# Kernel tuning notes

Hardware: AMD Instinct MI355X
Metric: run time of the kernel (lower is better)

The kernel has to match this reference:

```python
import jax, jax.numpy as jnp
import numpy as np

SIDE = 64; EMB = 16; CH = 64; K = 64; V = 64; L = 8
N = SIDE * SIDE

def _pos_table(side, d):
    pe = np.array([[p / np.power(10000, 2 * (j // 2) / d) for j in range(d)]
                   if p != 0 else np.zeros(d) for p in range(side)])
    pe[1:, 0::2] = np.sin(pe[1:, 0::2])
    pe[1:, 1::2] = np.cos(pe[1:, 1::2])
    return pe.astype(np.float32)  # [side, d]

def _pos_emb():
    # Replicates torch .view(1, emb, side, 1): plain reshape of [side, emb] -> [emb, side]
    t = _pos_table(SIDE, EMB).reshape(EMB, SIDE)
    xe = np.broadcast_to(t[:, :, None], (EMB, SIDE, SIDE))
    ye = np.broadcast_to(t[:, None, :], (EMB, SIDE, SIDE))
    return jnp.asarray(np.concatenate([xe, ye], 0).reshape(1, 2 * EMB, N))

def _conv_mask():
    # CausalConv mask, see_center=False, 5x5: zero center pixel onward in center row, and all rows below
    m = np.ones((CH, 3, 5, 5), np.float32)
    m[:, :, 2, 2:] = 0.0
    m[:, :, 3:, :] = 0.0
    return jnp.asarray(m)

def _lrelu(x):
    return jnp.where(x >= 0, x, 0.01 * x)  # LeakyReLU(0.01)

def _bn(x, g, b, eps=1e-5):
    # training-mode batch norm (biased variance), channel axis = 1
    axes = (0,) + tuple(range(2, x.ndim))
    m = jnp.mean(x, axes, keepdims=True)
    var = jnp.mean((x - m) ** 2, axes, keepdims=True)
    sh = (1, -1) + (1,) * (x.ndim - 2)
    return g.reshape(sh) * (x - m) / jnp.sqrt(var + eps) + b.reshape(sh)

def _cv1(w, b, x):
    # 1x1 Conv1d: [O,I] x [B,I,N] -> [B,O,N]
    return jnp.einsum('oi,bin->bon', w, x) + b[:, None]

def reference(x, conv_w, conv_b, bn0_g, bn0_b, q_w, q_b, fk_w, fk_b, ck_w, ck_b,
              fv_w, fv_b, cv_w, cv_b, bn_g, bn_b, out_w, out_b):
    B = x.shape[0]
    pos = jnp.broadcast_to(_pos_emb(), (B, 2 * EMB, N))
    mask = jnp.tril(jnp.ones((N, N), jnp.float32))

    # masked causal conv input layer + BN + LeakyReLU
    w = conv_w * _conv_mask()
    h = jax.lax.conv_general_dilated(x, w, (1, 1), [(2, 2), (2, 2)],
                                     dimension_numbers=('NCHW', 'OIHW', 'NCHW'))
    h = h + conv_b[None, :, None, None]
    h = _lrelu(_bn(h, bn0_g, bn0_b)).reshape(B, CH, N)

    k0 = jnp.zeros((B, K, N), x.dtype)
    v0 = jnp.zeros((B, V, N), x.dtype)
    inv_sqrt_k = 1.0 / jnp.sqrt(jnp.float32(K))

    def layer(carry, p):
        h, k, v = carry
        qw, qb, fkw, fkb, ckw, ckb, fvw, fvb, cvw, cvb, g, bb = p
        x0 = jnp.concatenate([h, pos], 1)            # [B, CH+32, N]
        x0k = jnp.concatenate([x0, k], 1)            # [B, 160, N]
        x0v = jnp.concatenate([x0, v], 1)
        fk = jax.nn.sigmoid(_cv1(fkw, fkb, x0k))
        ck = _lrelu(_cv1(ckw, ckb, x0k))
        k_new = fk * k + ck                          # highway-gated persistent K
        fv = jax.nn.sigmoid(_cv1(fvw, fvb, x0v))
        cv_ = _lrelu(_cv1(cvw, cvb, x0v))
        v_new = fv * v + cv_
        q = _lrelu(_cv1(qw, qb, x0))                 # [B, K, N]
        attn = jnp.einsum('bkn,bkm->bnm', q, k) * inv_sqrt_k  # uses OLD k
        attn = attn * mask + (1.0 - mask) * (-10000.0)
        attn = jax.nn.softmax(attn, axis=-1) * mask
        out1 = jnp.einsum('bnm,bvm->bvn', attn, v)   # uses OLD v; [B, V, N]
        # original code computes fc(out1) but discards it (out2 overwritten)
        h2 = _lrelu(_bn(out1, g, bb))
        return (h2, k_new, v_new), None

    params = (q_w, q_b, fk_w, fk_b, ck_w, ck_b, fv_w, fv_b, cv_w, cv_b, bn_g, bn_b)
    (h, k, v), _ = jax.lax.scan(layer, (h, k0, v0), params)

    out = jnp.einsum('oi,bin->bon', out_w, h) + out_b[None, :, None]
    return out.reshape(B, out_w.shape[0], SIDE, SIDE)

def setup_inputs() -> dict:
    key = jax.random.key(0)
    ks = jax.random.split(key, 12)
    s = 0.05
    return {
        'x': jax.random.normal(ks[0], (2, 3, 64, 64), jnp.float32),
        'conv_w': jax.random.normal(ks[1], (CH, 3, 5, 5), jnp.float32) * s,
        'conv_b': jnp.zeros((CH,), jnp.float32),
        'bn0_g': jnp.ones((CH,), jnp.float32),
        'bn0_b': jnp.zeros((CH,), jnp.float32),
        'q_w': jax.random.normal(ks[2], (L, K, CH + 2 * EMB), jnp.float32) * s,
        'q_b': jnp.zeros((L, K), jnp.float32),
        'fk_w': jax.random.normal(ks[3], (L, K, CH + K + 2 * EMB), jnp.float32) * s,
        'fk_b': jnp.zeros((L, K), jnp.float32),
        'ck_w': jax.random.normal(ks[4], (L, K, CH + K + 2 * EMB), jnp.float32) * s,
        'ck_b': jnp.zeros((L, K), jnp.float32),
        'fv_w': jax.random.normal(ks[5], (L, V, CH + V + 2 * EMB), jnp.float32) * s,
        'fv_b': jnp.zeros((L, V), jnp.float32),
        'cv_w': jax.random.normal(ks[6], (L, V, CH + V + 2 * EMB), jnp.float32) * s,
        'cv_b': jnp.zeros((L, V), jnp.float32),
        'bn_g': jnp.ones((L, CH), jnp.float32),
        'bn_b': jnp.zeros((L, CH), jnp.float32),
        'out_w': jax.random.normal(ks[7], (100, V), jnp.float32) * s,
        'out_b': jnp.zeros((100,), jnp.float32),
    }
```

## Files before the change

kernel.cpp:

```cpp
#include <hip/hip_runtime.h>

#define NPIX 4096
#define CHN  64

typedef __attribute__((ext_vector_type(8))) short short8;
typedef __attribute__((ext_vector_type(8))) unsigned short ushort8;
typedef __attribute__((ext_vector_type(4))) unsigned short ushort4v;
typedef __attribute__((ext_vector_type(4))) float f32x4;

__device__ __forceinline__ float lrelu_(float x){ return x >= 0.f ? x : 0.01f*x; }

__device__ __forceinline__ unsigned short f2bf(float x){
  union { float f; unsigned u; } v; v.f = x;
  unsigned r = v.u + 0x7FFF + ((v.u >> 16) & 1);
  return (unsigned short)(r >> 16);
}
__device__ __forceinline__ float bf2f(unsigned short h){
  union { unsigned u; float f; } v; v.u = ((unsigned)h) << 16;
  return v.f;
}

__global__ void pos_kernel(float* __restrict__ pos){
  int idx = blockIdx.x*256 + threadIdx.x;
  int c = idx >> 12;
  int n = idx & (NPIX-1);
  int bcoord = (c < 16) ? (n >> 6) : (n & 63);
  int a = (c < 16) ? c : (c - 16);
  int flat = a*64 + bcoord;
  int p = flat >> 4;
  int j = flat & 15;
  float val = 0.f;
  if (p != 0){
    float ex = (float)(j & ~1) * (1.f/16.f);
    float w = powf(10000.f, -ex);
    float ang = (float)p * w;
    val = (j & 1) ? cosf(ang) : sinf(ang);
  }
  pos[idx] = val;
}

__global__ void wtr_kernel(const float* __restrict__ qw, const float* __restrict__ fkw,
                           const float* __restrict__ ckw, const float* __restrict__ fvw,
                           const float* __restrict__ cvw, const float* __restrict__ convw,
                           float* __restrict__ wt){
  int idx = blockIdx.x*256 + threadIdx.x;
  if (idx >= 381632) return;
  if (idx < 49152){
    int l = idx / 6144, r = idx % 6144, i = r >> 6, o = r & 63;
    wt[idx] = qw[(l*64 + o)*96 + i];
  } else if (idx < 376832){
    int e = idx - 49152;
    int mat = e / 81920, r = e % 81920;
    int l = r / 10240, rr = r % 10240, i = rr >> 6, o = rr & 63;
    const float* src = (mat==0) ? fkw : (mat==1) ? ckw : (mat==2) ? fvw : cvw;
    wt[idx] = src[(l*64 + o)*160 + i];
  } else {
    int e = idx - 376832;
    int o = e & 63, tap = e >> 6;
    int ci = tap / 25, r = tap % 25;
    wt[idx] = convw[(o*3 + ci)*25 + r];
  }
}

__global__ __launch_bounds__(256) void conv_in_kernel(const float* __restrict__ x,
                                                      const float* __restrict__ cwt,
                                                      const float* __restrict__ cb,
                                                      float* __restrict__ out){
  int t = threadIdx.x;
  int o = t & 63;
  int sub = t >> 6;
  int bid = blockIdx.x;
  int b = bid >> 10;
  int n = ((bid & 1023) << 2) + sub;
  int y = n >> 6, xx = n & 63;
  float acc = cb[o];
  #pragma unroll
  for (int ci=0; ci<3; ++ci){
    const float* xp = x + ((b*3+ci)<<12);
    #pragma unroll
    for (int ky=0; ky<3; ++ky){
      int yy = y + ky - 2;
      if (yy < 0) continue;
      int nk = (ky==2) ? 2 : 5;
      #pragma unroll
      for (int kx=0; kx<5; ++kx){
        if (kx >= nk) break;
        int xc = xx + kx - 2;
        if (xc < 0 || xc > 63) continue;
        acc += xp[(yy<<6) + xc] * cwt[(ci*25 + ky*5 + kx)*64 + o];
      }
    }
  }
  out[(b*CHN+o)*NPIX + n] = acc;
}

__global__ __launch_bounds__(1024) void bn_stats_kernel(const float* __restrict__ xin,
                                                        float* __restrict__ stats){
  int c = blockIdx.x;
  int t = threadIdx.x;
  float s = 0.f, ss = 0.f;
  #pragma unroll
  for (int it=0; it<8; ++it){
    int idx = t + it*1024;
    float v = xin[(((idx>>12))*CHN + c)*NPIX + (idx & (NPIX-1))];
    s += v; ss += v*v;
  }
  #pragma unroll
  for (int o=1; o<64; o<<=1){ s += __shfl_xor(s,o); ss += __shfl_xor(ss,o); }
  __shared__ float ps[16], pq[16];
  if ((t & 63) == 0){ ps[t>>6] = s; pq[t>>6] = ss; }
  __syncthreads();
  if (t == 0){
    float S=0.f, Q=0.f;
    #pragma unroll
    for (int i=0;i<16;++i){ S += ps[i]; Q += pq[i]; }
    float mu = S*(1.f/8192.f);
    float var = Q*(1.f/8192.f) - mu*mu;
    var = fmaxf(var, 0.f);
    stats[c*2]   = mu;
    stats[c*2+1] = rsqrtf(var + 1e-5f);
  }
}

__global__ void bn_apply_kernel(const float* __restrict__ xin, const float* __restrict__ stats,
                                const float* __restrict__ g, const float* __restrict__ bb,
                                float* __restrict__ hout){
  int idx = blockIdx.x*256 + threadIdx.x;
  int e = idx << 2;
  int c = (e >> 12) & 63;
  float mu = stats[c*2], rstd = stats[c*2+1];
  float gain = g[c]*rstd;
  float beta = bb[c] - gain*mu;
  float4 v = *(const float4*)(xin + e);
  float4 r;
  r.x = lrelu_(gain*v.x + beta);
  r.y = lrelu_(gain*v.y + beta);
  r.z = lrelu_(gain*v.z + beta);
  r.w = lrelu_(gain*v.w + beta);
  *(float4*)(hout + e) = r;
}

__global__ __launch_bounds__(256) void bn_apply2_kernel(const float* __restrict__ xin,
                                                        const float* __restrict__ psum,
                                                        const float* __restrict__ psq,
                                                        const float* __restrict__ g,
                                                        const float* __restrict__ bb,
                                                        float* __restrict__ hout){
  int bid = blockIdx.x;
  int ebase = bid << 10;
  int c = (ebase >> 12) & 63;
  int t = threadIdx.x;
  float s = psum[c*256 + t];
  float q = psq[c*256 + t];
  #pragma unroll
  for (int o=1; o<64; o<<=1){ s += __shfl_xor(s,o); q += __shfl_xor(q,o); }
  __shared__ float as[4], aq[4];
  if ((t & 63) == 0){ as[t>>6] = s; aq[t>>6] = q; }
  __syncthreads();
  float S = as[0]+as[1]+as[2]+as[3];
  float Q = aq[0]+aq[1]+aq[2]+aq[3];
  float mu = S*(1.f/8192.f);
  float var = fmaxf(Q*(1.f/8192.f) - mu*mu, 0.f);
  float rstd = rsqrtf(var + 1e-5f);
  float gain = g[c]*rstd;
  float beta = bb[c] - gain*mu;
  float4 v = *(const float4*)(xin + ebase + t*4);
  float4 r;
  r.x = lrelu_(gain*v.x + beta);
  r.y = lrelu_(gain*v.y + beta);
  r.z = lrelu_(gain*v.z + beta);
  r.w = lrelu_(gain*v.w + beta);
  *(float4*)(hout + ebase + t*4) = r;
}

__global__ __launch_bounds__(256) void cv1_kernel(
    const float* __restrict__ hbuf, const float* __restrict__ pos,
    const float* __restrict__ kold, const float* __restrict__ vold,
    const float* __restrict__ qwt,
    const float* __restrict__ fkwt, const float* __restrict__ ckwt,
    const float* __restrict__ fvwt, const float* __restrict__ cvwt,
    const float* __restrict__ qbi,  const float* __restrict__ fkb,
    const float* __restrict__ ckb,  const float* __restrict__ fvb,
    const float* __restrict__ cvb,
    unsigned short* __restrict__ qh, unsigned short* __restrict__ ql,
    float* __restrict__ knew, unsigned short* __restrict__ khn, unsigned short* __restrict__ kln,
    float* __restrict__ vnew, unsigned short* __restrict__ vhTn, unsigned short* __restrict__ vlTn)
{
  int t = threadIdx.x;
  int o  = t & 63;
  int wv = t >> 6;
  int b    = blockIdx.x >> 8;
  int tile = blockIdx.x & 255;
  int n0 = tile*16 + wv*4;

  const float* hb = hbuf + b*CHN*NPIX + n0;
  const float* kb = kold + b*CHN*NPIX + n0;
  const float* vb = vold + b*CHN*NPIX + n0;
  const float* pb = pos + n0;

  auto load4 = [&](const float* p, float* dst){
    float4 a = *(const float4*)p;
    dst[0]=a.x; dst[1]=a.y; dst[2]=a.z; dst[3]=a.w;
  };

  float x[4];
  long obase = (long)(b*CHN+o)*NPIX + n0;
  size_t nbase = ((size_t)b*NPIX + n0)*64 + o;

  {
    float aq[4];
    float bias = qbi[o];
    #pragma unroll
    for (int j=0;j<4;++j) aq[j]=bias;
    #pragma unroll 4
    for (int i=0;i<64;++i){
      load4(hb + i*NPIX, x);
      float w = qwt[i*64 + o];
      #pragma unroll
      for (int j=0;j<4;++j) aq[j] += w*x[j];
    }
    #pragma unroll 4
    for (int i=0;i<32;++i){
      load4(pb + i*NPIX, x);
      float w = qwt[(64+i)*64 + o];
      #pragma unroll
      for (int j=0;j<4;++j) aq[j] += w*x[j];
    }
    #pragma unroll
    for (int j=0;j<4;++j){
      float v = lrelu_(aq[j]) * 0.125f;
      unsigned short hb16 = f2bf(v);
      qh[nbase + (size_t)j*64] = hb16;
      ql[nbase + (size_t)j*64] = f2bf(v - bf2f(hb16));
    }
  }

  {
    float af[4], ac[4];
    float bf = fkb[o], bc = ckb[o];
    #pragma unroll
    for (int j=0;j<4;++j){ af[j]=bf; ac[j]=bc; }
    #pragma unroll 4
    for (int i=0;i<64;++i){
      load4(hb + i*NPIX, x);
      float wf = fkwt[i*64+o], wc = ckwt[i*64+o];
      #pragma unroll
      for (int j=0;j<4;++j){ af[j] += wf*x[j]; ac[j] += wc*x[j]; }
    }
    #pragma unroll 4
    for (int i=0;i<32;++i){
      load4(pb + i*NPIX, x);
      float wf = fkwt[(64+i)*64+o], wc = ckwt[(64+i)*64+o];
      #pragma unroll
      for (int j=0;j<4;++j){ af[j] += wf*x[j]; ac[j] += wc*x[j]; }
    }
    #pragma unroll 4
    for (int i=0;i<64;++i){
      load4(kb + i*NPIX, x);
      float wf = fkwt[(96+i)*64+o], wc = ckwt[(96+i)*64+o];
      #pragma unroll
      for (int j=0;j<4;++j){ af[j] += wf*x[j]; ac[j] += wc*x[j]; }
    }
    float kv[4];
    load4(kb + o*NPIX, kv);
    #pragma unroll
    for (int j=0;j<4;++j){
      float fk = 1.f/(1.f+__expf(-af[j]));
      float kn = fk*kv[j] + lrelu_(ac[j]);
      knew[obase+j] = kn;
      unsigned short hb16 = f2bf(kn);
      khn[nbase + (size_t)j*64] = hb16;
      kln[nbase + (size_t)j*64] = f2bf(kn - bf2f(hb16));
    }
  }

  {
    float af[4], ac[4];
    float bf = fvb[o], bc = cvb[o];
    #pragma unroll
    for (int j=0;j<4;++j){ af[j]=bf; ac[j]=bc; }
    #pragma unroll 4
    for (int i=0;i<64;++i){
      load4(hb + i*NPIX, x);
      float wf = fvwt[i*64+o], wc = cvwt[i*64+o];
      #pragma unroll
      for (int j=0;j<4;++j){ af[j] += wf*x[j]; ac[j] += wc*x[j]; }
    }
    #pragma unroll 4
    for (int i=0;i<32;++i){
      load4(pb + i*NPIX, x);
      float wf = fvwt[(64+i)*64+o], wc = cvwt[(64+i)*64+o];
      #pragma unroll
      for (int j=0;j<4;++j){ af[j] += wf*x[j]; ac[j] += wc*x[j]; }
    }
    #pragma unroll 4
    for (int i=0;i<64;++i){
      load4(vb + i*NPIX, x);
      float wf = fvwt[(96+i)*64+o], wc = cvwt[(96+i)*64+o];
      #pragma unroll
      for (int j=0;j<4;++j){ af[j] += wf*x[j]; ac[j] += wc*x[j]; }
    }
    float vv[4];
    load4(vb + o*NPIX, vv);
    ushort4v vph, vpl;
    #pragma unroll
    for (int j=0;j<4;++j){
      float fv = 1.f/(1.f+__expf(-af[j]));
      float vn = fv*vv[j] + lrelu_(ac[j]);
      vnew[obase+j] = vn;
      unsigned short hb16 = f2bf(vn);
      vph[j] = hb16;
      vpl[j] = f2bf(vn - bf2f(hb16));
    }
    *(ushort4v*)(vhTn + ((size_t)(b*CHN+o))*NPIX + n0) = vph;
    *(ushort4v*)(vlTn + ((size_t)(b*CHN+o))*NPIX + n0) = vpl;
  }
}

__global__ __launch_bounds__(128) void attn_mfma(
    const unsigned short* __restrict__ qhg, const unsigned short* __restrict__ qlg,
    const unsigned short* __restrict__ khg, const unsigned short* __restrict__ klg,
    const unsigned short* __restrict__ vhg, const unsigned short* __restrict__ vlg,
    float* __restrict__ part)
{
  int bid = 639 - (int)blockIdx.x;
  int b = 0, id = bid;
  if (id >= 320){ b = 1; id -= 320; }
  int pidx = bid;
  int rem = id, k = 0;
  while (rem >= 32*(k+1)){ rem -= 32*(k+1); ++k; }
  int rt    = 32*k + rem/(k+1);
  int chunk = rem - (rem/(k+1))*(k+1);

  int C0  = chunk << 10;
  int end = min(C0 + 1024, rt*32 + 32);
  int nt  = (end - C0 + 63) >> 6;

  int t = threadIdx.x;
  int w = t >> 6;
  int l = t & 63;
  int r = l & 15;
  int g = l >> 4;
  int n_g = rt*32 + w*16 + r;

  __shared__ __align__(16) char KH[8192], KL[8192];
  __shared__ __align__(16) char VH[8192], VL[8192];
  __shared__ __align__(16) char PH[2][2048], PL[2][2048];

  const unsigned short* qhp = qhg + (size_t)b*NPIX*64;
  const unsigned short* qlp = qlg + (size_t)b*NPIX*64;
  const unsigned short* khp = khg + (size_t)b*NPIX*64;
  const unsigned short* klp = klg + (size_t)b*NPIX*64;
  const unsigned short* vhp = vhg + (size_t)b*CHN*NPIX;
  const unsigned short* vlp = vlg + (size_t)b*CHN*NPIX;

  short8 qh0 = *(const short8*)(qhp + (size_t)n_g*64 + 8*g);
  short8 qh1 = *(const short8*)(qhp + (size_t)n_g*64 + 8*g + 32);
  short8 ql0 = *(const short8*)(qlp + (size_t)n_g*64 + 8*g);
  short8 ql1 = *(const short8*)(qlp + (size_t)n_g*64 + 8*g + 32);

  int srow[4], scc8[4], soff[4];
  #pragma unroll
  for (int p=0; p<4; ++p){
    int slot = t + (p<<7);
    int row = slot >> 3, cc = slot & 7;
    srow[p] = row; scc8[p] = cc*8;
    soff[p] = row*128 + ((cc ^ (row & 7)) << 4);
  }

  ushort8 rkh[4], rkl[4], rvh[4], rvl[4];
  auto issue = [&](int m0){
    #pragma unroll
    for (int p=0; p<4; ++p){
      rkh[p] = *(const ushort8*)(khp + (size_t)(m0+srow[p])*64 + scc8[p]);
      rkl[p] = *(const ushort8*)(klp + (size_t)(m0+srow[p])*64 + scc8[p]);
      rvh[p] = *(const ushort8*)(vhp + (size_t)srow[p]*NPIX + m0 + scc8[p]);
      rvl[p] = *(const ushort8*)(vlp + (size_t)srow[p]*NPIX + m0 + scc8[p]);
    }
  };

  f32x4 zero4 = {0.f,0.f,0.f,0.f};
  f32x4 oacc[4];
  #pragma unroll
  for (int vf=0; vf<4; ++vf) oacc[vf] = zero4;
  float m_run = -1e30f, l_run = 0.f;

  int nmax_w = rt*32 + w*16 + 15;

  issue(C0);
  for (int ti=0; ti<nt; ++ti){
    int m0 = C0 + (ti<<6);
    __syncthreads();
    #pragma unroll
    for (int p=0; p<4; ++p){
      *(ushort8*)(KH + soff[p]) = rkh[p];
      *(ushort8*)(KL + soff[p]) = rkl[p];
      *(ushort8*)(VH + soff[p]) = rvh[p];
      *(ushort8*)(VL + soff[p]) = rvl[p];
    }
    __syncthreads();
    if (ti+1 < nt) issue(m0 + 64);

    if (m0 <= nmax_w){
      f32x4 sf[4];
      #pragma unroll
      for (int mf=0; mf<4; ++mf) sf[mf] = zero4;
      #pragma unroll
      for (int kc=0; kc<2; ++kc){
        short8 qfh = kc ? qh1 : qh0;
        short8 qfl = kc ? ql1 : ql0;
        int ch = ((g + 4*kc) ^ (r & 7)) << 4;
        #pragma unroll
        for (int mf=0; mf<4; ++mf){
          int ro = (16*mf + r)*128;
          short8 ah = *(const short8*)(KH + ro + ch);
          short8 al = *(const short8*)(KL + ro + ch);
          sf[mf] = __builtin_amdgcn_mfma_f32_16x16x32_bf16(ah, qfh, sf[mf], 0,0,0);
          sf[mf] = __builtin_amdgcn_mfma_f32_16x16x32_bf16(al, qfh, sf[mf], 0,0,0);
          sf[mf] = __builtin_amdgcn_mfma_f32_16x16x32_bf16(ah, qfl, sf[mf], 0,0,0);
        }
      }
      float pv[16];
      float mx = -1e30f;
      #pragma unroll
      for (int mf=0; mf<4; ++mf){
        #pragma unroll
        for (int q2=0; q2<4; ++q2){
          int mg = m0 + 16*mf + 4*g + q2;
          float s = sf[mf][q2];
          s = (mg <= n_g) ? s : -1e30f;
          pv[mf*4+q2] = s;
          mx = fmaxf(mx, s);
        }
      }
      mx = fmaxf(mx, __shfl_xor(mx, 16));
      mx = fmaxf(mx, __shfl_xor(mx, 32));
      float m_new = fmaxf(m_run, mx);
      float alpha = __expf(m_run - m_new);
      float ps = 0.f;
      #pragma unroll
      for (int i=0; i<16; ++i){ pv[i] = __expf(pv[i] - m_new); ps += pv[i]; }
      ps += __shfl_xor(ps, 16);
      ps += __shfl_xor(ps, 32);
      l_run = l_run*alpha + ps;
      m_run = m_new;

      #pragma unroll
      for (int mf=0; mf<4; ++mf){
        unsigned short h_[4], l_[4];
        #pragma unroll
        for (int q2=0; q2<4; ++q2){
          float xv = pv[mf*4+q2];
          h_[q2] = f2bf(xv);
          l_[q2] = f2bf(xv - bf2f(h_[q2]));
        }
        int addr = r*128 + ((((g>>1) + 2*mf) ^ (r & 7)) << 4) + ((g&1)<<3);
        uint2 wh = make_uint2((unsigned)h_[0] | ((unsigned)h_[1]<<16),
                              (unsigned)h_[2] | ((unsigned)h_[3]<<16));
        uint2 wl = make_uint2((unsigned)l_[0] | ((unsigned)l_[1]<<16),
                              (unsigned)l_[2] | ((unsigned)l_[3]<<16));
        *(uint2*)(PH[w] + addr) = wh;
        *(uint2*)(PL[w] + addr) = wl;
      }
      #pragma unroll
      for (int vf=0; vf<4; ++vf) oacc[vf] *= alpha;

      #pragma unroll
      for (int kc=0; kc<2; ++kc){
        int ch = ((g + 4*kc) ^ (r & 7)) << 4;
        short8 pfh = *(const short8*)(PH[w] + r*128 + ch);
        short8 pfl = *(const short8*)(PL[w] + r*128 + ch);
        #pragma unroll
        for (int vf=0; vf<4; ++vf){
          int ro = (16*vf + r)*128;
          short8 ah = *(const short8*)(VH + ro + ch);
          short8 al = *(const short8*)(VL + ro + ch);
          oacc[vf] = __builtin_amdgcn_mfma_f32_16x16x32_bf16(ah, pfh, oacc[vf], 0,0,0);
          oacc[vf] = __builtin_amdgcn_mfma_f32_16x16x32_bf16(al, pfh, oacc[vf], 0,0,0);
          oacc[vf] = __builtin_amdgcn_mfma_f32_16x16x32_bf16(ah, pfl, oacc[vf], 0,0,0);
        }
      }
    }
  }

  float* pacc = part + (size_t)pidx * 2112;
  int nl = w*16 + r;
  #pragma unroll
  for (int vf=0; vf<4; ++vf)
    *(f32x4*)(pacc + nl*64 + 16*vf + 4*g) = oacc[vf];
  if (g == 0){
    pacc[2048 + nl*2]   = m_run;
    pacc[2048 + nl*2+1] = l_run;
  }
}

__global__ __launch_bounds__(256) void attn_combine(const float* __restrict__ part,
                                                    float* __restrict__ out1,
                                                    float* __restrict__ psum,
                                                    float* __restrict__ psq){
  int bid = blockIdx.x;
  int b = bid >> 7, rt = bid & 127;
  int k = rt >> 5;
  int nch = k + 1;
  int base = b*320 + 16*k*(k+1) + (rt - 32*k)*nch;

  int t = threadIdx.x;
  int nl = t & 31, vq = t >> 5;

  float M = -1e30f;
  #pragma unroll
  for (int c=0; c<4; ++c)
    if (c < nch) M = fmaxf(M, part[(size_t)(base+c)*2112 + 2048 + nl*2]);

  float L = 0.f;
  float val[8];
  #pragma unroll
  for (int jj=0; jj<8; ++jj) val[jj] = 0.f;
  #pragma unroll
  for (int c=0; c<4; ++c){
    if (c < nch){
      const float* pa = part + (size_t)(base+c)*2112;
      float wgt = __expf(pa[2048 + nl*2] - M);
      L += pa[2048 + nl*2 + 1] * wgt;
      #pragma unroll
      for (int jj=0; jj<8; ++jj) val[jj] += wgt * pa[nl*64 + vq*8 + jj];
    }
  }
  float invL = 1.f / L;
  float s[8], q[8];
  #pragma unroll
  for (int jj=0; jj<8; ++jj){
    float v = val[jj]*invL;
    out1[((size_t)b*CHN + vq*8 + jj)*NPIX + rt*32 + nl] = v;
    s[jj] = v; q[jj] = v*v;
  }
  #pragma unroll
  for (int o2=1; o2<32; o2<<=1){
    #pragma unroll
    for (int jj=0; jj<8; ++jj){
      s[jj] += __shfl_xor(s[jj], o2);
      q[jj] += __shfl_xor(q[jj], o2);
    }
  }
  if (nl == 0){
    #pragma unroll
    for (int jj=0; jj<8; ++jj){
      int c = vq*8 + jj;
      psum[c*256 + bid] = s[jj];
      psq [c*256 + bid] = q[jj];
    }
  }
}

__global__ __launch_bounds__(256) void final_kernel(const float* __restrict__ h,
                                                    const float* __restrict__ ow,
                                                    const float* __restrict__ ob,
                                                    float* __restrict__ out){
  int idx = blockIdx.x*256 + threadIdx.x;
  int b  = idx / 409600;
  int r  = idx - b*409600;
  int oc = r >> 12;
  int n  = r & (NPIX-1);
  const float* hp = h + (size_t)b*CHN*NPIX + n;
  const float* wp = ow + oc*64;
  float acc = ob[oc];
  #pragma unroll
  for (int v=0; v<64; ++v) acc += wp[v]*hp[(size_t)v*NPIX];
  out[idx] = acc;
}

extern "C" void kernel_launch(void* const* d_in, const int* in_sizes, int n_in,
                              void* d_out, int out_size, void* d_ws, size_t ws_size,
                              hipStream_t stream){
  const float* x     = (const float*)d_in[0];
  const float* convw = (const float*)d_in[1];
  const float* convb = (const float*)d_in[2];
  const float* bn0g  = (const float*)d_in[3];
  const float* bn0b  = (const float*)d_in[4];
  const float* qw    = (const float*)d_in[5];
  const float* qbias = (const float*)d_in[6];
  const float* fkw   = (const float*)d_in[7];
  const float* fkb   = (const float*)d_in[8];
  const float* ckw   = (const float*)d_in[9];
  const float* ckb   = (const float*)d_in[10];
  const float* fvw   = (const float*)d_in[11];
  const float* fvb   = (const float*)d_in[12];
  const float* cvw   = (const float*)d_in[13];
  const float* cvb   = (const float*)d_in[14];
  const float* bng   = (const float*)d_in[15];
  const float* bnb   = (const float*)d_in[16];
  const float* ow    = (const float*)d_in[17];
  const float* ob    = (const float*)d_in[18];

  const size_t TEN = (size_t)2*CHN*NPIX;
  const size_t BFU = TEN/2;
  float* ws   = (float*)d_ws;
  float* pos  = ws;
  float* h    = pos + 32*NPIX;
  float* k0   = h  + TEN;
  float* k1   = k0 + TEN;
  float* v0   = k1 + TEN;
  float* v1   = v0 + TEN;
  float* o1   = v1 + TEN;
  float* stats = o1 + TEN;
  float* psum = stats + 128;
  float* psq  = psum + 64*256;
  float* wt   = psq + 64*256;
  float* bfb  = wt + 381632;
  unsigned short* qh  = (unsigned short*)(bfb);
  unsigned short* ql  = (unsigned short*)(bfb + BFU);
  unsigned short* kh0 = (unsigned short*)(bfb + 2*BFU);
  unsigned short* kh1 = (unsigned short*)(bfb + 3*BFU);
  unsigned short* kl0 = (unsigned short*)(bfb + 4*BFU);
  unsigned short* kl1 = (unsigned short*)(bfb + 5*BFU);
  unsigned short* vh0 = (unsigned short*)(bfb + 6*BFU);
  unsigned short* vh1 = (unsigned short*)(bfb + 7*BFU);
  unsigned short* vl0 = (unsigned short*)(bfb + 8*BFU);
  unsigned short* vl1 = (unsigned short*)(bfb + 9*BFU);
  float* part = bfb + 10*BFU;

  hipMemsetAsync(k0, 0, TEN*sizeof(float), stream);
  hipMemsetAsync(v0, 0, TEN*sizeof(float), stream);
  hipMemsetAsync(kh0, 0, TEN*2, stream);
  hipMemsetAsync(kl0, 0, TEN*2, stream);
  hipMemsetAsync(vh0, 0, TEN*2, stream);
  hipMemsetAsync(vl0, 0, TEN*2, stream);

  pos_kernel<<<512,256,0,stream>>>(pos);
  wtr_kernel<<<1491,256,0,stream>>>(qw, fkw, ckw, fvw, cvw, convw, wt);
  conv_in_kernel<<<2048,256,0,stream>>>(x, wt + 376832, convb, o1);
  bn_stats_kernel<<<64,1024,0,stream>>>(o1, stats);
  bn_apply_kernel<<<512,256,0,stream>>>(o1, stats, bn0g, bn0b, h);

  float* kfp[2] = {k0,k1};
  float* vfp[2] = {v0,v1};
  unsigned short* khb[2] = {kh0,kh1};
  unsigned short* klb[2] = {kl0,kl1};
  unsigned short* vhb[2] = {vh0,vh1};
  unsigned short* vlb[2] = {vl0,vl1};
  for (int l=0; l<8; ++l){
    float* kold = kfp[l&1]; float* knew = kfp[(l+1)&1];
    float* vold = vfp[l&1]; float* vnew = vfp[(l+1)&1];
    cv1_kernel<<<512,256,0,stream>>>(h, pos, kold, vold,
        wt + l*6144,
        wt + 49152 + l*10240,
        wt + 49152 + 81920 + l*10240,
        wt + 49152 + 2*81920 + l*10240,
        wt + 49152 + 3*81920 + l*10240,
        qbias + l*64, fkb + l*64, ckb + l*64, fvb + l*64, cvb + l*64,
        qh, ql,
        knew, khb[(l+1)&1], klb[(l+1)&1],
        vnew, vhb[(l+1)&1], vlb[(l+1)&1]);
    attn_mfma<<<640,128,0,stream>>>(qh, ql, khb[l&1], klb[l&1], vhb[l&1], vlb[l&1], part);
    attn_combine<<<256,256,0,stream>>>(part, o1, psum, psq);
    bn_apply2_kernel<<<512,256,0,stream>>>(o1, psum, psq, bng + l*64, bnb + l*64, h);
  }
  final_kernel<<<3200,256,0,stream>>>(h, ow, ob, (float*)d_out);
}
```

Before: 823.0 us.

## Retile causal attention to 128-query blocks with 32x32 bf16 MFMA

The attention kernel now runs 256-thread blocks that each cover 128 query rows, one 32-row slice per wave, over 512-key chunks. It switches from 16x16x32 to 32x32x16 bf16 MFMA, packs P to bf16 with v_cvt_pk_bf16_f32, and the combine kernel's partial indexing is updated to match. The intent is more reuse of each staged K/V tile per load and fewer softmax shuffles. In exchange the grid shrinks from 640 to 288 blocks, which may hurt load balance and occupancy, and register and LDS pressure rise. Separately, the o1 buffer is dropped and h is updated in place by the conv, combine and BN steps, saving a buffer of memory traffic.

```diff
diff --git a/kernel.cpp b/kernel.cpp
--- a/kernel.cpp
+++ b/kernel.cpp
@@ -7,6 +7,7 @@
 typedef __attribute__((ext_vector_type(8))) unsigned short ushort8;
 typedef __attribute__((ext_vector_type(4))) unsigned short ushort4v;
 typedef __attribute__((ext_vector_type(4))) float f32x4;
+typedef __attribute__((ext_vector_type(16))) float f32x16;
 
 __device__ __forceinline__ float lrelu_(float x){ return x >= 0.f ? x : 0.01f*x; }
 
@@ -18,6 +19,9 @@
 __device__ __forceinline__ float bf2f(unsigned short h){
   union { unsigned u; float f; } v; v.u = ((unsigned)h) << 16;
   return v.f;
+}
+__device__ __forceinline__ float asf_(unsigned u){
+  union { unsigned u; float f; } v; v.u = u; return v.f;
 }
 
 __global__ void pos_kernel(float* __restrict__ pos){
@@ -140,12 +144,11 @@
   *(float4*)(hout + e) = r;
 }
 
-__global__ __launch_bounds__(256) void bn_apply2_kernel(const float* __restrict__ xin,
+__global__ __launch_bounds__(256) void bn_apply2_kernel(float* __restrict__ hbuf,
                                                         const float* __restrict__ psum,
                                                         const float* __restrict__ psq,
                                                         const float* __restrict__ g,
-                                                        const float* __restrict__ bb,
-                                                        float* __restrict__ hout){
+                                                        const float* __restrict__ bb){
   int bid = blockIdx.x;
   int ebase = bid << 10;
   int c = (ebase >> 12) & 63;
@@ -164,13 +167,13 @@
   float rstd = rsqrtf(var + 1e-5f);
   float gain = g[c]*rstd;
   float beta = bb[c] - gain*mu;
-  float4 v = *(const float4*)(xin + ebase + t*4);
+  float4 v = *(const float4*)(hbuf + ebase + t*4);
   float4 r;
   r.x = lrelu_(gain*v.x + beta);
   r.y = lrelu_(gain*v.y + beta);
   r.z = lrelu_(gain*v.z + beta);
   r.w = lrelu_(gain*v.w + beta);
-  *(float4*)(hout + ebase + t*4) = r;
+  *(float4*)(hbuf + ebase + t*4) = r;
 }
 
 __global__ __launch_bounds__(256) void cv1_kernel(
@@ -317,35 +320,37 @@
   }
 }
 
-__global__ __launch_bounds__(128) void attn_mfma(
+__global__ __launch_bounds__(256) void attn_mfma(
     const unsigned short* __restrict__ qhg, const unsigned short* __restrict__ qlg,
     const unsigned short* __restrict__ khg, const unsigned short* __restrict__ klg,
     const unsigned short* __restrict__ vhg, const unsigned short* __restrict__ vlg,
     float* __restrict__ part)
 {
-  int bid = 639 - (int)blockIdx.x;
+  int bid = 287 - (int)blockIdx.x;
   int b = 0, id = bid;
-  if (id >= 320){ b = 1; id -= 320; }
+  if (id >= 144){ b = 1; id -= 144; }
   int pidx = bid;
   int rem = id, k = 0;
-  while (rem >= 32*(k+1)){ rem -= 32*(k+1); ++k; }
-  int rt    = 32*k + rem/(k+1);
+  while (rem >= 4*(k+1)){ rem -= 4*(k+1); ++k; }
+  int rtg   = 4*k + rem/(k+1);
   int chunk = rem - (rem/(k+1))*(k+1);
 
-  int C0  = chunk << 10;
-  int end = min(C0 + 1024, rt*32 + 32);
+  int C0  = chunk << 9;
+  int end = min(C0 + 512, rtg*128 + 128);
   int nt  = (end - C0 + 63) >> 6;
 
   int t = threadIdx.x;
   int w = t >> 6;
   int l = t & 63;
-  int r = l & 15;
-  int g = l >> 4;
-  int n_g = rt*32 + w*16 + r;
+  int q = l & 31;
+  int hi = l >> 5;
+  int qbase = rtg*128 + w*32;
+  int n_g = qbase + q;
+  int nmax_w = qbase + 31;
 
   __shared__ __align__(16) char KH[8192], KL[8192];
   __shared__ __align__(16) char VH[8192], VL[8192];
-  __shared__ __align__(16) char PH[2][2048], PL[2][2048];
+  __shared__ __align__(16) char PH[4][4096], PL[4][4096];
 
   const unsigned short* qhp = qhg + (size_t)b*NPIX*64;
   const unsigned short* qlp = qlg + (size_t)b*NPIX*64;
@@ -354,24 +359,25 @@
   const unsigned short* vhp = vhg + (size_t)b*CHN*NPIX;
   const unsigned short* vlp = vlg + (size_t)b*CHN*NPIX;
 
-  short8 qh0 = *(const short8*)(qhp + (size_t)n_g*64 + 8*g);
-  short8 qh1 = *(const short8*)(qhp + (size_t)n_g*64 + 8*g + 32);
-  short8 ql0 = *(const short8*)(qlp + (size_t)n_g*64 + 8*g);
-  short8 ql1 = *(const short8*)(qlp + (size_t)n_g*64 + 8*g + 32);
-
-  int srow[4], scc8[4], soff[4];
-  #pragma unroll
-  for (int p=0; p<4; ++p){
-    int slot = t + (p<<7);
+  short8 qhf[4], qlf[4];
+  #pragma unroll
+  for (int kc=0; kc<4; ++kc){
+    qhf[kc] = *(const short8*)(qhp + (size_t)n_g*64 + kc*16 + hi*8);
+    qlf[kc] = *(const short8*)(qlp + (size_t)n_g*64 + kc*16 + hi*8);
+  }
+
+  int srow[2], scc8[2], soff[2];
+  #pragma unroll
+  for (int p=0; p<2; ++p){
+    int slot = t + (p<<8);
     int row = slot >> 3, cc = slot & 7;
     srow[p] = row; scc8[p] = cc*8;
     soff[p] = row*128 + ((cc ^ (row & 7)) << 4);
   }
-
-  ushort8 rkh[4], rkl[4], rvh[4], rvl[4];
+  ushort8 rkh[2], rkl[2], rvh[2], rvl[2];
   auto issue = [&](int m0){
     #pragma unroll
-    for (int p=0; p<4; ++p){
+    for (int p=0; p<2; ++p){
       rkh[p] = *(const ushort8*)(khp + (size_t)(m0+srow[p])*64 + scc8[p]);
       rkl[p] = *(const ushort8*)(klp + (size_t)(m0+srow[p])*64 + scc8[p]);
       rvh[p] = *(const ushort8*)(vhp + (size_t)srow[p]*NPIX + m0 + scc8[p]);
@@ -379,20 +385,20 @@
     }
   };
 
-  f32x4 zero4 = {0.f,0.f,0.f,0.f};
-  f32x4 oacc[4];
-  #pragma unroll
-  for (int vf=0; vf<4; ++vf) oacc[vf] = zero4;
+  f32x16 oacc0, oacc1;
+  #pragma unroll
+  for (int i=0; i<16; ++i){ oacc0[i]=0.f; oacc1[i]=0.f; }
   float m_run = -1e30f, l_run = 0.f;
 
-  int nmax_w = rt*32 + w*16 + 15;
+  char* phw = PH[w];
+  char* plw = PL[w];
 
   issue(C0);
   for (int ti=0; ti<nt; ++ti){
     int m0 = C0 + (ti<<6);
     __syncthreads();
     #pragma unroll
-    for (int p=0; p<4; ++p){
+    for (int p=0; p<2; ++p){
       *(ushort8*)(KH + soff[p]) = rkh[p];
       *(ushort8*)(KL + soff[p]) = rkl[p];
       *(ushort8*)(VH + soff[p]) = rvh[p];
@@ -402,95 +408,110 @@
     if (ti+1 < nt) issue(m0 + 64);
 
     if (m0 <= nmax_w){
-      f32x4 sf[4];
-      #pragma unroll
-      for (int mf=0; mf<4; ++mf) sf[mf] = zero4;
-      #pragma unroll
-      for (int kc=0; kc<2; ++kc){
-        short8 qfh = kc ? qh1 : qh0;
-        short8 qfl = kc ? ql1 : ql0;
-        int ch = ((g + 4*kc) ^ (r & 7)) << 4;
-        #pragma unroll
-        for (int mf=0; mf<4; ++mf){
-          int ro = (16*mf + r)*128;
-          short8 ah = *(const short8*)(KH + ro + ch);
-          short8 al = *(const short8*)(KL + ro + ch);
-          sf[mf] = __builtin_amdgcn_mfma_f32_16x16x32_bf16(ah, qfh, sf[mf], 0,0,0);
-          sf[mf] = __builtin_amdgcn_mfma_f32_16x16x32_bf16(al, qfh, sf[mf], 0,0,0);
-          sf[mf] = __builtin_amdgcn_mfma_f32_16x16x32_bf16(ah, qfl, sf[mf], 0,0,0);
-        }
+      f32x16 sf0, sf1;
+      #pragma unroll
+      for (int i=0; i<16; ++i){ sf0[i]=0.f; sf1[i]=0.f; }
+      #pragma unroll
+      for (int kc=0; kc<4; ++kc){
+        int off0 = q*128 + (((2*kc + hi) ^ (q & 7)) << 4);
+        short8 ah0 = *(const short8*)(KH + off0);
+        short8 al0 = *(const short8*)(KL + off0);
+        short8 ah1 = *(const short8*)(KH + off0 + 4096);
+        short8 al1 = *(const short8*)(KL + off0 + 4096);
+        sf0 = __builtin_amdgcn_mfma_f32_32x32x16_bf16(ah0, qhf[kc], sf0, 0,0,0);
+        sf1 = __builtin_amdgcn_mfma_f32_32x32x16_bf16(ah1, qhf[kc], sf1, 0,0,0);
+        sf0 = __builtin_amdgcn_mfma_f32_32x32x16_bf16(al0, qhf[kc], sf0, 0,0,0);
+        sf1 = __builtin_amdgcn_mfma_f32_32x32x16_bf16(al1, qhf[kc], sf1, 0,0,0);
+        sf0 = __builtin_amdgcn_mfma_f32_32x32x16_bf16(ah0, qlf[kc], sf0, 0,0,0);
+        sf1 = __builtin_amdgcn_mfma_f32_32x32x16_bf16(ah1, qlf[kc], sf1, 0,0,0);
       }
-      float pv[16];
       float mx = -1e30f;
       #pragma unroll
-      for (int mf=0; mf<4; ++mf){
-        #pragma unroll
-        for (int q2=0; q2<4; ++q2){
-          int mg = m0 + 16*mf + 4*g + q2;
-          float s = sf[mf][q2];
-          s = (mg <= n_g) ? s : -1e30f;
-          pv[mf*4+q2] = s;
-          mx = fmaxf(mx, s);
-        }
+      for (int r=0; r<16; ++r){
+        int mg0 = m0 + (r&3) + 8*(r>>2) + 4*hi;
+        float s0 = (mg0 <= n_g) ? sf0[r] : -1e30f;
+        float s1 = (mg0 + 32 <= n_g) ? sf1[r] : -1e30f;
+        sf0[r] = s0; sf1[r] = s1;
+        mx = fmaxf(mx, fmaxf(s0, s1));
       }
-      mx = fmaxf(mx, __shfl_xor(mx, 16));
       mx = fmaxf(mx, __shfl_xor(mx, 32));
       float m_new = fmaxf(m_run, mx);
       float alpha = __expf(m_run - m_new);
       float ps = 0.f;
       #pragma unroll
-      for (int i=0; i<16; ++i){ pv[i] = __expf(pv[i] - m_new); ps += pv[i]; }
-      ps += __shfl_xor(ps, 16);
+      for (int r=0; r<16; ++r){
+        float e0 = __expf(sf0[r] - m_new);
+        float e1 = __expf(sf1[r] - m_new);
+        sf0[r] = e0; sf1[r] = e1;
+        ps += e0 + e1;
+      }
       ps += __shfl_xor(ps, 32);
       l_run = l_run*alpha + ps;
       m_run = m_new;
 
       #pragma unroll
-      for (int mf=0; mf<4; ++mf){
-        unsigned short h_[4], l_[4];
+      for (int mf=0; mf<2; ++mf){
         #pragma unroll
-        for (int q2=0; q2<4; ++q2){
-          float xv = pv[mf*4+q2];
-          h_[q2] = f2bf(xv);
-          l_[q2] = f2bf(xv - bf2f(h_[q2]));
-        }
-        int addr = r*128 + ((((g>>1) + 2*mf) ^ (r & 7)) << 4) + ((g&1)<<3);
-        uint2 wh = make_uint2((unsigned)h_[0] | ((unsigned)h_[1]<<16),
-                              (unsigned)h_[2] | ((unsigned)h_[3]<<16));
-        uint2 wl = make_uint2((unsigned)l_[0] | ((unsigned)l_[1]<<16),
-                              (unsigned)l_[2] | ((unsigned)l_[3]<<16));
-        *(uint2*)(PH[w] + addr) = wh;
-        *(uint2*)(PL[w] + addr) = wl;
-      }
-      #pragma unroll
-      for (int vf=0; vf<4; ++vf) oacc[vf] *= alpha;
-
-      #pragma unroll
-      for (int kc=0; kc<2; ++kc){
-        int ch = ((g + 4*kc) ^ (r & 7)) << 4;
-        short8 pfh = *(const short8*)(PH[w] + r*128 + ch);
-        short8 pfl = *(const short8*)(PL[w] + r*128 + ch);
-        #pragma unroll
-        for (int vf=0; vf<4; ++vf){
-          int ro = (16*vf + r)*128;
-          short8 ah = *(const short8*)(VH + ro + ch);
-          short8 al = *(const short8*)(VL + ro + ch);
-          oacc[vf] = __builtin_amdgcn_mfma_f32_16x16x32_bf16(ah, pfh, oacc[vf], 0,0,0);
-          oacc[vf] = __builtin_amdgcn_mfma_f32_16x16x32_bf16(al, pfh, oacc[vf], 0,0,0);
-          oacc[vf] = __builtin_amdgcn_mfma_f32_16x16x32_bf16(ah, pfl, oacc[vf], 0,0,0);
+        for (int qd=0; qd<4; ++qd){
+          float a0 = mf ? sf1[4*qd]   : sf0[4*qd];
+          float a1 = mf ? sf1[4*qd+1] : sf0[4*qd+1];
+          float a2 = mf ? sf1[4*qd+2] : sf0[4*qd+2];
+          float a3 = mf ? sf1[4*qd+3] : sf0[4*qd+3];
+          unsigned wh0, wh1;
+          asm("v_cvt_pk_bf16_f32 %0, %1, %2" : "=v"(wh0) : "v"(a0), "v"(a1));
+          asm("v_cvt_pk_bf16_f32 %0, %1, %2" : "=v"(wh1) : "v"(a2), "v"(a3));
+          float l0 = a0 - asf_(wh0 << 16);
+          float l1 = a1 - asf_(wh0 & 0xffff0000u);
+          float l2 = a2 - asf_(wh1 << 16);
+          float l3 = a3 - asf_(wh1 & 0xffff0000u);
+          unsigned wl0, wl1;
+          asm("v_cvt_pk_bf16_f32 %0, %1, %2" : "=v"(wl0) : "v"(l0), "v"(l1));
+          asm("v_cvt_pk_bf16_f32 %0, %1, %2" : "=v"(wl1) : "v"(l2), "v"(l3));
+          int mchunk = 4*mf + qd;
+          int boff = q*128 + ((mchunk ^ (q & 7)) << 4) + (hi << 3);
+          *(uint2*)(phw + boff) = make_uint2(wh0, wh1);
+          *(uint2*)(plw + boff) = make_uint2(wl0, wl1);
         }
       }
-    }
-  }
-
-  float* pacc = part + (size_t)pidx * 2112;
-  int nl = w*16 + r;
-  #pragma unroll
-  for (int vf=0; vf<4; ++vf)
-    *(f32x4*)(pacc + nl*64 + 16*vf + 4*g) = oacc[vf];
-  if (g == 0){
-    pacc[2048 + nl*2]   = m_run;
-    pacc[2048 + nl*2+1] = l_run;
+      #pragma unroll
+      for (int i=0; i<16; ++i){ oacc0[i] *= alpha; oacc1[i] *= alpha; }
+
+      #pragma unroll
+      for (int kc=0; kc<4; ++kc){
+        int poff = q*128 + (((2*kc + hi) ^ (q & 7)) << 4);
+        short8 pfh = *(const short8*)(phw + poff);
+        short8 pfl = *(const short8*)(plw + poff);
+        short8 vh0 = *(const short8*)(VH + poff);
+        short8 vl0 = *(const short8*)(VL + poff);
+        short8 vh1 = *(const short8*)(VH + poff + 4096);
+        short8 vl1 = *(const short8*)(VL + poff + 4096);
+        oacc0 = __builtin_amdgcn_mfma_f32_32x32x16_bf16(vh0, pfh, oacc0, 0,0,0);
+        oacc1 = __builtin_amdgcn_mfma_f32_32x32x16_bf16(vh1, pfh, oacc1, 0,0,0);
+        oacc0 = __builtin_amdgcn_mfma_f32_32x32x16_bf16(vl0, pfh, oacc0, 0,0,0);
+        oacc1 = __builtin_amdgcn_mfma_f32_32x32x16_bf16(vl1, pfh, oacc1, 0,0,0);
+        oacc0 = __builtin_amdgcn_mfma_f32_32x32x16_bf16(vh0, pfl, oacc0, 0,0,0);
+        oacc1 = __builtin_amdgcn_mfma_f32_32x32x16_bf16(vh1, pfl, oacc1, 0,0,0);
+      }
+    }
+  }
+
+  float* pacc = part + (size_t)pidx * 8448;
+  #pragma unroll
+  for (int vf=0; vf<2; ++vf){
+    #pragma unroll
+    for (int qd=0; qd<4; ++qd){
+      int vd = 32*vf + 8*qd + 4*hi;
+      f32x4 vv;
+      vv.x = vf ? oacc1[4*qd]   : oacc0[4*qd];
+      vv.y = vf ? oacc1[4*qd+1] : oacc0[4*qd+1];
+      vv.z = vf ? oacc1[4*qd+2] : oacc0[4*qd+2];
+      vv.w = vf ? oacc1[4*qd+3] : oacc0[4*qd+3];
+      *(f32x4*)(pacc + (size_t)(w*32 + q)*64 + vd) = vv;
+    }
+  }
+  if (l < 32){
+    pacc[8192 + (w*32 + l)*2]     = m_run;
+    pacc[8192 + (w*32 + l)*2 + 1] = l_run;
   }
 }
 
@@ -500,30 +521,32 @@
                                                     float* __restrict__ psq){
   int bid = blockIdx.x;
   int b = bid >> 7, rt = bid & 127;
-  int k = rt >> 5;
-  int nch = k + 1;
-  int base = b*320 + 16*k*(k+1) + (rt - 32*k)*nch;
+  int rtg = rt >> 2;
+  int k2 = rtg >> 2;
+  int nch = k2 + 1;
+  int base = b*144 + 2*k2*(k2+1) + (rtg & 3)*(k2+1);
 
   int t = threadIdx.x;
   int nl = t & 31, vq = t >> 5;
+  int row128 = (rt & 3)*32 + nl;
 
   float M = -1e30f;
   #pragma unroll
-  for (int c=0; c<4; ++c)
-    if (c < nch) M = fmaxf(M, part[(size_t)(base+c)*2112 + 2048 + nl*2]);
+  for (int c=0; c<8; ++c)
+    if (c < nch) M = fmaxf(M, part[(size_t)(base+c)*8448 + 8192 + row128*2]);
 
   float L = 0.f;
   float val[8];
   #pragma unroll
   for (int jj=0; jj<8; ++jj) val[jj] = 0.f;
   #pragma unroll
-  for (int c=0; c<4; ++c){
+  for (int c=0; c<8; ++c){
     if (c < nch){
-      const float* pa = part + (size_t)(base+c)*2112;
-      float wgt = __expf(pa[2048 + nl*2] - M);
-      L += pa[2048 + nl*2 + 1] * wgt;
-      #pragma unroll
-      for (int jj=0; jj<8; ++jj) val[jj] += wgt * pa[nl*64 + vq*8 + jj];
+      const float* pa = part + (size_t)(base+c)*8448;
+      float wgt = __expf(pa[8192 + row128*2] - M);
+      L += pa[8192 + row128*2 + 1] * wgt;
+      #pragma unroll
+      for (int jj=0; jj<8; ++jj) val[jj] += wgt * pa[row128*64 + vq*8 + jj];
     }
   }
   float invL = 1.f / L;
@@ -601,8 +624,7 @@
   float* k1   = k0 + TEN;
   float* v0   = k1 + TEN;
   float* v1   = v0 + TEN;
-  float* o1   = v1 + TEN;
-  float* stats = o1 + TEN;
+  float* stats = v1 + TEN;
   float* psum = stats + 128;
   float* psq  = psum + 64*256;
   float* wt   = psq + 64*256;
@@ -628,9 +650,9 @@
 
   pos_kernel<<<512,256,0,stream>>>(pos);
   wtr_kernel<<<1491,256,0,stream>>>(qw, fkw, ckw, fvw, cvw, convw, wt);
-  conv_in_kernel<<<2048,256,0,stream>>>(x, wt + 376832, convb, o1);
-  bn_stats_kernel<<<64,1024,0,stream>>>(o1, stats);
-  bn_apply_kernel<<<512,256,0,stream>>>(o1, stats, bn0g, bn0b, h);
+  conv_in_kernel<<<2048,256,0,stream>>>(x, wt + 376832, convb, h);
+  bn_stats_kernel<<<64,1024,0,stream>>>(h, stats);
+  bn_apply_kernel<<<512,256,0,stream>>>(h, stats, bn0g, bn0b, h);
 
   float* kfp[2] = {k0,k1};
   float* vfp[2] = {v0,v1};
@@ -651,9 +673,9 @@
         qh, ql,
         knew, khb[(l+1)&1], klb[(l+1)&1],
         vnew, vhb[(l+1)&1], vlb[(l+1)&1]);
-    attn_mfma<<<640,128,0,stream>>>(qh, ql, khb[l&1], klb[l&1], vhb[l&1], vlb[l&1], part);
-    attn_combine<<<256,256,0,stream>>>(part, o1, psum, psq);
-    bn_apply2_kernel<<<512,256,0,stream>>>(o1, psum, psq, bng + l*64, bnb + l*64, h);
+    attn_mfma<<<288,256,0,stream>>>(qh, ql, khb[l&1], klb[l&1], vhb[l&1], vlb[l&1], part);
+    attn_combine<<<256,256,0,stream>>>(part, h, psum, psq);
+    bn_apply2_kernel<<<512,256,0,stream>>>(h, psum, psq, bng + l*64, bnb + l*64);
   }
   final_kernel<<<3200,256,0,stream>>>(h, ow, ob, (float*)d_out);
 }
```

Measured after the change: 847.6 us. +3.0%, slower.
